# Optimization experiments

Measured on AMD Instinct MI355X. Metric: run time of the kernel, lower is better.

Reference implementation:

```python
import jax, jax.numpy as jnp
import numpy as np

D_MODEL, D_STATE, D_CONV, DT_RANK = 512, 64, 4, 32


def setup_inputs() -> dict:
    key = jax.random.key(0)
    ks = jax.random.split(key, 8)
    Bsz, L = 2, 2048
    s = lambda k, shape: jax.random.normal(k, shape, jnp.float32) * 0.02
    return {
        "x": jax.random.normal(ks[0], (Bsz, L, D_MODEL), jnp.float32),
        "in_proj_w": s(ks[1], (D_MODEL, 2 * D_MODEL)),
        "in_proj_b": jnp.zeros((2 * D_MODEL,), jnp.float32),
        "conv_w": s(ks[2], (D_MODEL, 1, D_CONV)),  # depthwise: [C_out, C_in/groups=1, K]
        "conv_b": jnp.zeros((D_MODEL,), jnp.float32),
        "x_proj_w": s(ks[3], (D_MODEL, DT_RANK + 2 * D_STATE)),
        "x_proj_b": jnp.zeros((DT_RANK + 2 * D_STATE,), jnp.float32),
        "dt_proj_w": s(ks[4], (DT_RANK, D_MODEL)),
        "dt_proj_b": jnp.zeros((D_MODEL,), jnp.float32),
        "A_log": jnp.log(jnp.broadcast_to(
            jnp.arange(1, D_STATE + 1, dtype=jnp.float32), (D_MODEL, D_STATE))),
        "B_param": jax.random.normal(ks[5], (D_MODEL, D_STATE), jnp.float32),
        "C_param": jax.random.normal(ks[6], (D_MODEL, D_STATE), jnp.float32),
        "D_param": jnp.ones((D_MODEL,), jnp.float32),
    }


def reference(x, in_proj_w, in_proj_b, conv_w, conv_b, x_proj_w, x_proj_b,
              dt_proj_w, dt_proj_b, A_log, B_param, C_param, D_param):
    Bsz, L, _ = x.shape
    # in_proj -> split into (x, z)
    xz = x @ in_proj_w + in_proj_b                       # [B, L, 2D]
    xc, z = jnp.split(xz, 2, axis=-1)                    # each [B, L, D]
    # depthwise causal conv1d, padding=K-1 both sides, truncate to L (as in torch)
    y = jax.lax.conv_general_dilated(
        xc.transpose(0, 2, 1), conv_w, window_strides=(1,),
        padding=[(D_CONV - 1, D_CONV - 1)],
        dimension_numbers=("NCH", "OIH", "NCH"),
        feature_group_count=D_MODEL)                     # [B, D, L+K-1]
    xc = (y + conv_b[None, :, None])[:, :, :L].transpose(0, 2, 1)  # [B, L, D]
    # selective parameters
    xp = xc @ x_proj_w + x_proj_b                        # [B, L, dt_rank + 2N]
    dt, Bp, Cp = jnp.split(xp, [DT_RANK, DT_RANK + D_STATE], axis=-1)
    dt = jax.nn.softplus(dt @ dt_proj_w + dt_proj_b)     # [B, L, D]
    A = -jnp.exp(A_log)                                  # [D, N]

    def step(h, ins):
        dt_t, Bp_t, Cp_t, u_t = ins                      # [B,D],[B,N],[B,N],[B,D]
        A_d = jnp.exp(dt_t[..., None] * A)               # [B, D, N]
        B_d = dt_t[..., None] * (B_param * Bp_t[:, None, :])
        h = A_d * h + B_d * u_t[..., None]               # [B, D, N]
        y_t = jnp.sum((C_param * Cp_t[:, None, :]) * h, axis=-1)  # [B, D]
        return h, y_t

    h0 = jnp.zeros((Bsz, D_MODEL, D_STATE), x.dtype)
    xs = (dt.transpose(1, 0, 2), Bp.transpose(1, 0, 2),
          Cp.transpose(1, 0, 2), xc.transpose(1, 0, 2))
    _, ys = jax.lax.scan(step, h0, xs)                   # ys: [L, B, D]
    y = ys.transpose(1, 0, 2) + D_param * xc             # skip connection
    return y * jax.nn.silu(z)                            # gated output [B, L, D]
```

## Files before the change

### kernel.cpp

```cpp
#include <hip/hip_runtime.h>
#include <hip/hip_bf16.h>

#define BSZ 2
#define SEQL 2048
#define DM 512
#define DST 64
#define DCONV 4
#define DTR 32
#define NROWS (BSZ * SEQL)

#define NC 32
#define CL 64

#define XPD_LD 640

typedef unsigned short u16;
typedef short bf16x8 __attribute__((ext_vector_type(8)));
typedef float f32x4 __attribute__((ext_vector_type(4)));

#if __has_builtin(__builtin_amdgcn_exp2f)
#define EXP2(x) __builtin_amdgcn_exp2f(x)
#else
#define EXP2(x) exp2f(x)
#endif
#if __has_builtin(__builtin_amdgcn_logf)
#define LOG2(x) __builtin_amdgcn_logf(x)
#else
#define LOG2(x) log2f(x)
#endif

__device__ __forceinline__ u16 f2bf(float f) {
  unsigned u = __float_as_uint(f);
  return (u16)((u + 0x7FFFu + ((u >> 16) & 1u)) >> 16);
}
__device__ __forceinline__ float bf2f(u16 h) {
  return __uint_as_float(((unsigned)h) << 16);
}

__device__ __forceinline__ void gload_lds16(const u16* g, u16* l) {
  __builtin_amdgcn_global_load_lds(
      (const __attribute__((address_space(1))) void*)(const void*)g,
      (__attribute__((address_space(3))) void*)(void*)l, 16, 0, 0);
}

__global__ __launch_bounds__(256) void split_x_kernel(
    const float* __restrict__ x, u16* __restrict__ hi, u16* __restrict__ lo) {
  int idx = (blockIdx.x * 256 + threadIdx.x) * 4;
  float4 v = *(const float4*)(x + idx);
  ushort4 h, l;
  h.x = f2bf(v.x); l.x = f2bf(v.x - bf2f(h.x));
  h.y = f2bf(v.y); l.y = f2bf(v.y - bf2f(h.y));
  h.z = f2bf(v.z); l.z = f2bf(v.z - bf2f(h.z));
  h.w = f2bf(v.w); l.w = f2bf(v.w - bf2f(h.w));
  *(ushort4*)(hi + idx) = h;
  *(ushort4*)(lo + idx) = l;
}

__global__ __launch_bounds__(256) void split_w_kernel(
    const float* __restrict__ W, u16* __restrict__ Wt_hi,
    u16* __restrict__ Wt_lo) {
  __shared__ u16 shi[32][33], slo[32][33];
  const int n0 = blockIdx.x * 32;
  const int k0 = blockIdx.y * 32;
  const int i = threadIdx.x >> 5;
  const int j = threadIdx.x & 31;
#pragma unroll
  for (int r = 0; r < 4; ++r) {
    int k = i + r * 8;
    float v = W[(size_t)(k0 + k) * 1024 + n0 + j];
    u16 h = f2bf(v);
    shi[k][j] = h;
    slo[k][j] = f2bf(v - bf2f(h));
  }
  __syncthreads();
#pragma unroll
  for (int r = 0; r < 4; ++r) {
    int n = i + r * 8;
    Wt_hi[(size_t)(n0 + n) * 512 + k0 + j] = shi[j][n];
    Wt_lo[(size_t)(n0 + n) * 512 + k0 + j] = slo[j][n];
  }
}

__global__ __launch_bounds__(256) void w_combine_kernel(
    const float* __restrict__ xw, const float* __restrict__ dw,
    u16* __restrict__ Wt_hi, u16* __restrict__ Wt_lo) {
  int idx = blockIdx.x * 256 + threadIdx.x;
  int r = idx >> 9;
  int k = idx & 511;
  float v;
  if (r < 128) {
    v = xw[(size_t)k * 160 + 32 + r];
  } else {
    int d = r - 128;
    float s = 0.f;
#pragma unroll
    for (int j = 0; j < DTR; ++j) s += xw[(size_t)k * 160 + j] * dw[(size_t)j * DM + d];
    v = s;
  }
  u16 h = f2bf(v);
  Wt_hi[idx] = h;
  Wt_lo[idx] = f2bf(v - bf2f(h));
}

__global__ __launch_bounds__(256) void bias_combine_kernel(
    const float* __restrict__ xb, const float* __restrict__ dw,
    const float* __restrict__ db, float* __restrict__ bias_c) {
  int r = blockIdx.x * 256 + threadIdx.x;
  if (r >= 640) return;
  float v;
  if (r < 128) {
    v = xb[32 + r];
  } else {
    int d = r - 128;
    float s = db[d];
#pragma unroll
    for (int j = 0; j < DTR; ++j) s += xb[j] * dw[(size_t)j * DM + d];
    v = s;
  }
  bias_c[r] = v;
}

__global__ __launch_bounds__(256) void mfma_split_gemm(
    const u16* __restrict__ A_hi, const u16* __restrict__ A_lo,
    const u16* __restrict__ Bt_hi, const u16* __restrict__ Bt_lo,
    const float* __restrict__ bias, float* __restrict__ C) {
  __shared__ alignas(16) u16 sAh[4096], sAl[4096], sBh[4096], sBl[4096];

  const int lane = threadIdx.x & 63;
  const int wv = threadIdx.x >> 6;
  const int bm = blockIdx.y * 128;
  const int bn = blockIdx.x * 128;
  const int fr = lane & 15;
  const int q = lane >> 4;

  const int st_rowc = lane >> 2;
  const int st_qd = lane & 3;

  const bf16x8 *pAh[4], *pAl[4], *pBh[4], *pBl[4];
#pragma unroll
  for (int t = 0; t < 4; ++t) {
    int ra = (wv >> 1) * 64 + t * 16 + fr;
    int ea = ra * 32 + ((q ^ ((ra >> 1) & 3)) * 8);
    pAh[t] = (const bf16x8*)(sAh + ea);
    pAl[t] = (const bf16x8*)(sAl + ea);
    int rb = (wv & 1) * 64 + t * 16 + fr;
    int eb = rb * 32 + ((q ^ ((rb >> 1) & 3)) * 8);
    pBh[t] = (const bf16x8*)(sBh + eb);
    pBl[t] = (const bf16x8*)(sBl + eb);
  }

  f32x4 zero = {0.f, 0.f, 0.f, 0.f};
  f32x4 acc[4][4];
#pragma unroll
  for (int i = 0; i < 4; ++i)
#pragma unroll
    for (int j = 0; j < 4; ++j) acc[i][j] = zero;

  auto stage = [&](int k0) {
#pragma unroll
    for (int i = 0; i < 2; ++i) {
      int c = wv + i * 4;
      int row = c * 16 + st_rowc;
      int qs = st_qd ^ ((row >> 1) & 3);
      size_t ga = (size_t)(bm + row) * 512 + k0 + qs * 8;
      size_t gb = (size_t)(bn + row) * 512 + k0 + qs * 8;
      gload_lds16(A_hi + ga, sAh + c * 512);
      gload_lds16(A_lo + ga, sAl + c * 512);
      gload_lds16(Bt_hi + gb, sBh + c * 512);
      gload_lds16(Bt_lo + gb, sBl + c * 512);
    }
  };

  stage(0);
  for (int kt = 0; kt < 16; ++kt) {
    __syncthreads();
    bf16x8 ah[4], al[4], bh[4], bl[4];
#pragma unroll
    for (int t = 0; t < 4; ++t) {
      ah[t] = *pAh[t];
      al[t] = *pAl[t];
      bh[t] = *pBh[t];
      bl[t] = *pBl[t];
    }
    __syncthreads();
    if (kt < 15) stage((kt + 1) * 32);
#pragma unroll
    for (int mi = 0; mi < 4; ++mi)
#pragma unroll
      for (int nj = 0; nj < 4; ++nj) {
        f32x4 a = acc[mi][nj];
        a = __builtin_amdgcn_mfma_f32_16x16x32_bf16(al[mi], bh[nj], a, 0, 0, 0);
        a = __builtin_amdgcn_mfma_f32_16x16x32_bf16(ah[mi], bl[nj], a, 0, 0, 0);
        a = __builtin_amdgcn_mfma_f32_16x16x32_bf16(ah[mi], bh[nj], a, 0, 0, 0);
        acc[mi][nj] = a;
      }
  }

#pragma unroll
  for (int mi = 0; mi < 4; ++mi) {
#pragma unroll
    for (int nj = 0; nj < 4; ++nj) {
      int row = bm + (wv >> 1) * 64 + mi * 16 + q * 4;
      int col = bn + (wv & 1) * 64 + nj * 16 + fr;
      float bs = bias[col];
#pragma unroll
      for (int e = 0; e < 4; ++e)
        C[(size_t)(row + e) * 1024 + col] = acc[mi][nj][e] + bs;
    }
  }
}

__global__ __launch_bounds__(256) void xpd_gemm_kernel(
    const u16* __restrict__ A_hi, const u16* __restrict__ A_lo,
    const u16* __restrict__ Bt_hi, const u16* __restrict__ Bt_lo,
    const float* __restrict__ bias, float* __restrict__ C) {
  __shared__ alignas(16) u16 sBh[64 * 512];
  __shared__ alignas(16) u16 sBl[64 * 512];

  const int lane = threadIdx.x & 63;
  const int wv = threadIdx.x >> 6;
  const int wr = wv >> 1;
  const int wc = wv & 1;
  const int bm = blockIdx.y * 128;
  const int bn = blockIdx.x * 64;
  const int fr = lane & 15;
  const int q = lane >> 4;

  {
    const int r0 = wv * 16;
#pragma unroll
    for (int i = 0; i < 16; ++i) {
      int r = r0 + i;
      size_t g = (size_t)(bn + r) * 512 + (size_t)(lane ^ (r & 7)) * 8;
      gload_lds16(Bt_hi + g, sBh + r * 512);
      gload_lds16(Bt_lo + g, sBl + r * 512);
    }
  }
  __syncthreads();

  size_t arow[4];
#pragma unroll
  for (int mi = 0; mi < 4; ++mi)
    arow[mi] = (size_t)(bm + wr * 64 + mi * 16 + fr) * 512;
  int bcol[2];
#pragma unroll
  for (int nj = 0; nj < 2; ++nj) bcol[nj] = wc * 32 + nj * 16 + fr;

  f32x4 zero = {0.f, 0.f, 0.f, 0.f};
  f32x4 acc[4][2];
#pragma unroll
  for (int i = 0; i < 4; ++i) {
    acc[i][0] = zero;
    acc[i][1] = zero;
  }

#pragma unroll 4
  for (int kt = 0; kt < 16; ++kt) {
    bf16x8 ah[4], al[4], bh[2], bl[2];
    const int kc = kt * 4 + q;
#pragma unroll
    for (int nj = 0; nj < 2; ++nj) {
      int off = bcol[nj] * 512 + ((kc ^ (bcol[nj] & 7)) * 8);
      bh[nj] = *(const bf16x8*)(sBh + off);
      bl[nj] = *(const bf16x8*)(sBl + off);
    }
#pragma unroll
    for (int mi = 0; mi < 4; ++mi) {
      size_t ga = arow[mi] + kt * 32 + q * 8;
      ah[mi] = *(const bf16x8*)(A_hi + ga);
      al[mi] = *(const bf16x8*)(A_lo + ga);
    }
#pragma unroll
    for (int mi = 0; mi < 4; ++mi)
#pragma unroll
      for (int nj = 0; nj < 2; ++nj) {
        f32x4 a = acc[mi][nj];
        a = __builtin_amdgcn_mfma_f32_16x16x32_bf16(al[mi], bh[nj], a, 0, 0, 0);
        a = __builtin_amdgcn_mfma_f32_16x16x32_bf16(ah[mi], bl[nj], a, 0, 0, 0);
        a = __builtin_amdgcn_mfma_f32_16x16x32_bf16(ah[mi], bh[nj], a, 0, 0, 0);
        acc[mi][nj] = a;
      }
  }

  const bool act = (bn >= 128);
#pragma unroll
  for (int mi = 0; mi < 4; ++mi) {
#pragma unroll
    for (int nj = 0; nj < 2; ++nj) {
      int row = bm + wr * 64 + mi * 16 + q * 4;
      int col = bn + wc * 32 + nj * 16 + fr;
      float bs = bias[col];
#pragma unroll
      for (int e = 0; e < 4; ++e) {
        float v = acc[mi][nj][e] + bs;
        if (act) {
          float sp = 0.6931471806f * LOG2(1.f + EXP2(v * 1.44269504f));
          v = (v > 20.f) ? v : sp;
        }
        C[(size_t)(row + e) * XPD_LD + col] = v;
      }
    }
  }
}

__global__ __launch_bounds__(256) void conv_split_kernel(
    const float* __restrict__ xz, const float* __restrict__ w,
    const float* __restrict__ cb, float* __restrict__ xc,
    u16* __restrict__ hi, u16* __restrict__ lo) {
  int idx4 = blockIdx.x * 256 + threadIdx.x;
  if (idx4 >= NROWS * DM / 4) return;
  const int d0 = (idx4 & (DM / 4 - 1)) * 4;
  const int row = idx4 >> 7;
  const int t = row & (SEQL - 1);

  float4 acc = *(const float4*)(cb + d0);
#pragma unroll
  for (int k = 0; k < DCONV; ++k) {
    int ts = t + k - (DCONV - 1);
    if (ts >= 0) {
      float4 v = *(const float4*)(xz + (size_t)(row + k - (DCONV - 1)) * (2 * DM) + d0);
      acc.x += w[(d0 + 0) * DCONV + k] * v.x;
      acc.y += w[(d0 + 1) * DCONV + k] * v.y;
      acc.z += w[(d0 + 2) * DCONV + k] * v.z;
      acc.w += w[(d0 + 3) * DCONV + k] * v.w;
    }
  }
  size_t o = (size_t)row * DM + d0;
  *(float4*)(xc + o) = acc;
  ushort4 h, l;
  h.x = f2bf(acc.x); l.x = f2bf(acc.x - bf2f(h.x));
  h.y = f2bf(acc.y); l.y = f2bf(acc.y - bf2f(h.y));
  h.z = f2bf(acc.z); l.z = f2bf(acc.z - bf2f(h.z));
  h.w = f2bf(acc.w); l.w = f2bf(acc.w - bf2f(h.w));
  *(ushort4*)(hi + o) = h;
  *(ushort4*)(lo + o) = l;
}

__global__ __launch_bounds__(256) void scan_phase1(
    const float* __restrict__ xpd, const float* __restrict__ xc,
    const float* __restrict__ A_log, const float* __restrict__ Bpar,
    float* __restrict__ hout, float* __restrict__ sdt_arr) {
  const int lane = threadIdx.x & 63;
  const int wid = (blockIdx.x << 2) + (threadIdx.x >> 6);
  const int ch = wid >> 5;
  const int c = wid & (NC - 1);
  const int b = ch >> 9;
  const int d = ch & (DM - 1);
  const int n = lane;

  const float aq = -__expf(A_log[d * DST + n]) * 1.44269504f;
  const float bpn = Bpar[d * DST + n];
  float h = 0.f, sdt = 0.f;

  const size_t row0 = (size_t)b * SEQL + (size_t)c * CL;
  const float* dtp = xpd + row0 * XPD_LD + 128 + d;
  const float* up = xc + row0 * DM + d;
  const float* bp = xpd + row0 * XPD_LD + n;

  for (int t0 = 0; t0 < CL; t0 += 4) {
    float dtv[4], uv[4], bpt[4];
#pragma unroll
    for (int j = 0; j < 4; ++j) {
      dtv[j] = dtp[(size_t)(t0 + j) * XPD_LD];
      uv[j] = up[(size_t)(t0 + j) * DM];
      bpt[j] = bp[(size_t)(t0 + j) * XPD_LD];
    }
#pragma unroll
    for (int j = 0; j < 4; ++j) {
      float Ad = EXP2(dtv[j] * aq);
      h = Ad * h + (bpn * bpt[j]) * (dtv[j] * uv[j]);
      sdt += dtv[j];
    }
  }
  hout[(size_t)wid * DST + n] = h;
  if (lane == 0) sdt_arr[wid] = sdt;
}

__global__ __launch_bounds__(256) void scan_phase2(
    const float* __restrict__ A_log, float* __restrict__ hout,
    const float* __restrict__ sdt_arr) {
  const int lane = threadIdx.x & 63;
  const int ch = (blockIdx.x << 2) + (threadIdx.x >> 6);
  const int d = ch & (DM - 1);
  const float aq = -__expf(A_log[d * DST + lane]) * 1.44269504f;

  float tmp[NC], pa[NC];
#pragma unroll
  for (int c = 0; c < NC; ++c) {
    tmp[c] = hout[((size_t)ch * NC + c) * DST + lane];
    pa[c] = EXP2(aq * sdt_arr[ch * NC + c]);
  }
  float h = 0.f;
#pragma unroll
  for (int c = 0; c < NC; ++c) {
    hout[((size_t)ch * NC + c) * DST + lane] = h;
    h = pa[c] * h + tmp[c];
  }
}

__global__ __launch_bounds__(256) void scan_phase3(
    const float* __restrict__ xpd, const float* __restrict__ xc,
    const float* __restrict__ xz,
    const float* __restrict__ A_log, const float* __restrict__ Bpar,
    const float* __restrict__ Cpar, const float* __restrict__ Dpar,
    const float* __restrict__ hin, float* __restrict__ out) {
  __shared__ float W[4][16][68];

  const int lane = threadIdx.x & 63;
  const int wave = threadIdx.x >> 6;
  const int wid = (blockIdx.x << 2) + wave;
  const int ch = wid >> 5;
  const int c = wid & (NC - 1);
  const int b = ch >> 9;
  const int d = ch & (DM - 1);
  const int n = lane;

  const float aq = -__expf(A_log[d * DST + n]) * 1.44269504f;
  const float bpn = Bpar[d * DST + n];
  const float cpn = Cpar[d * DST + n];
  const float Dd = Dpar[d];
  float h = hin[(size_t)wid * DST + n];

  const size_t row0 = (size_t)b * SEQL + (size_t)c * CL;
  const float* dtp = xpd + row0 * XPD_LD + 128 + d;
  const float* up = xc + row0 * DM + d;
  const float* bp = xpd + row0 * XPD_LD + n;
  const float* cp = xpd + row0 * XPD_LD + 64 + n;

  const int tt = lane & 15;
  const int q = lane >> 4;

  for (int t0 = 0; t0 < CL; t0 += 16) {
#pragma unroll
    for (int g = 0; g < 16; g += 4) {
      float dtv[4], uv[4], bpt[4], cpt[4];
#pragma unroll
      for (int j = 0; j < 4; ++j) {
        size_t t = (size_t)(t0 + g + j);
        dtv[j] = dtp[t * XPD_LD];
        uv[j] = up[t * DM];
        bpt[j] = bp[t * XPD_LD];
        cpt[j] = cp[t * XPD_LD];
      }
#pragma unroll
      for (int j = 0; j < 4; ++j) {
        float Ad = EXP2(dtv[j] * aq);
        h = Ad * h + (bpn * bpt[j]) * (dtv[j] * uv[j]);
        W[wave][g + j][n] = (cpn * cpt[j]) * h;
      }
    }
    const float4* wr = (const float4*)&W[wave][tt][q * 16];
    float s = 0.f;
#pragma unroll
    for (int k2 = 0; k2 < 4; ++k2) {
      float4 v = wr[k2];
      s += (v.x + v.y) + (v.z + v.w);
    }
    s += __shfl_xor(s, 16, 64);
    s += __shfl_xor(s, 32, 64);
    if (lane < 16) {
      size_t t = (size_t)(t0 + lane);
      float u = up[t * DM];
      float zz = xz[(row0 + t) * (2 * DM) + DM + d];
      float y = s + Dd * u;
      float sil = zz / (1.f + __expf(-zz));
      out[(row0 + t) * DM + d] = y * sil;
    }
  }
}

extern "C" void kernel_launch(void* const* d_in, const int* in_sizes, int n_in,
                              void* d_out, int out_size, void* d_ws,
                              size_t ws_size, hipStream_t stream) {
  const float* x = (const float*)d_in[0];
  const float* in_proj_w = (const float*)d_in[1];
  const float* in_proj_b = (const float*)d_in[2];
  const float* conv_w = (const float*)d_in[3];
  const float* conv_b = (const float*)d_in[4];
  const float* x_proj_w = (const float*)d_in[5];
  const float* x_proj_b = (const float*)d_in[6];
  const float* dt_proj_w = (const float*)d_in[7];
  const float* dt_proj_b = (const float*)d_in[8];
  const float* A_log = (const float*)d_in[9];
  const float* B_param = (const float*)d_in[10];
  const float* C_param = (const float*)d_in[11];
  const float* D_param = (const float*)d_in[12];
  float* out = (float*)d_out;

  float* ws = (float*)d_ws;
  float* xz = ws;
  float* xc = xz + (size_t)NROWS * 2 * DM;
  float* xpd = xc + (size_t)NROWS * DM;
  float* hout = xpd + (size_t)NROWS * XPD_LD;
  float* sdt = hout + (size_t)BSZ * DM * NC * DST;
  float* bias_c = sdt + (size_t)BSZ * DM * NC;
  u16* A_hi = (u16*)(bias_c + 1024);
  u16* A_lo = A_hi + (size_t)NROWS * DM;
  u16* Wt_in_hi = A_lo + (size_t)NROWS * DM;
  u16* Wt_in_lo = Wt_in_hi + (size_t)1024 * 512;
  u16* Wt_c_hi = Wt_in_lo + (size_t)1024 * 512;
  u16* Wt_c_lo = Wt_c_hi + (size_t)640 * 512;

  hipLaunchKernelGGL(split_x_kernel, dim3((NROWS * DM) / (256 * 4)), dim3(256),
                     0, stream, x, A_hi, A_lo);
  hipLaunchKernelGGL(split_w_kernel, dim3(32, 16), dim3(256), 0, stream,
                     in_proj_w, Wt_in_hi, Wt_in_lo);
  hipLaunchKernelGGL(w_combine_kernel, dim3((640 * 512) / 256), dim3(256), 0,
                     stream, x_proj_w, dt_proj_w, Wt_c_hi, Wt_c_lo);
  hipLaunchKernelGGL(bias_combine_kernel, dim3(3), dim3(256), 0, stream,
                     x_proj_b, dt_proj_w, dt_proj_b, bias_c);

  hipLaunchKernelGGL(mfma_split_gemm, dim3(1024 / 128, NROWS / 128),
                     dim3(256), 0, stream, A_hi, A_lo, Wt_in_hi, Wt_in_lo,
                     in_proj_b, xz);

  hipLaunchKernelGGL(conv_split_kernel, dim3((NROWS * DM / 4 + 255) / 256),
                     dim3(256), 0, stream, xz, conv_w, conv_b, xc, A_hi, A_lo);

  hipLaunchKernelGGL(xpd_gemm_kernel, dim3(640 / 64, NROWS / 128),
                     dim3(256), 0, stream, A_hi, A_lo, Wt_c_hi, Wt_c_lo,
                     bias_c, xpd);

  {
    dim3 grid((BSZ * DM * NC) / 4);
    hipLaunchKernelGGL(scan_phase1, grid, dim3(256), 0, stream,
                       xpd, xc, A_log, B_param, hout, sdt);
    hipLaunchKernelGGL(scan_phase2, dim3((BSZ * DM) / 4), dim3(256), 0, stream,
                       A_log, hout, sdt);
    hipLaunchKernelGGL(scan_phase3, grid, dim3(256), 0, stream,
                       xpd, xc, xz, A_log, B_param, C_param, D_param,
                       hout, out);
  }
}
```

Before: 247.4 us.

## Keep in_proj weight tile resident in LDS and stream A from global

Result: slower. 265.4 us (+7.3%).

```diff
diff --git a/kernel.cpp b/kernel.cpp
--- a/kernel.cpp
+++ b/kernel.cpp
@@ -120,74 +120,70 @@
   bias_c[r] = v;
 }
 
-__global__ __launch_bounds__(256) void mfma_split_gemm(
+__global__ __launch_bounds__(256) void in_proj_resident_kernel(
     const u16* __restrict__ A_hi, const u16* __restrict__ A_lo,
     const u16* __restrict__ Bt_hi, const u16* __restrict__ Bt_lo,
     const float* __restrict__ bias, float* __restrict__ C) {
-  __shared__ alignas(16) u16 sAh[4096], sAl[4096], sBh[4096], sBl[4096];
+  __shared__ alignas(16) u16 sBh[64 * 512];
+  __shared__ alignas(16) u16 sBl[64 * 512];
 
   const int lane = threadIdx.x & 63;
   const int wv = threadIdx.x >> 6;
+  const int wr = wv >> 1;
+  const int wc = wv & 1;
   const int bm = blockIdx.y * 128;
-  const int bn = blockIdx.x * 128;
+  const int bn = blockIdx.x * 64;
   const int fr = lane & 15;
   const int q = lane >> 4;
 
-  const int st_rowc = lane >> 2;
-  const int st_qd = lane & 3;
-
-  const bf16x8 *pAh[4], *pAl[4], *pBh[4], *pBl[4];
-#pragma unroll
-  for (int t = 0; t < 4; ++t) {
-    int ra = (wv >> 1) * 64 + t * 16 + fr;
-    int ea = ra * 32 + ((q ^ ((ra >> 1) & 3)) * 8);
-    pAh[t] = (const bf16x8*)(sAh + ea);
-    pAl[t] = (const bf16x8*)(sAl + ea);
-    int rb = (wv & 1) * 64 + t * 16 + fr;
-    int eb = rb * 32 + ((q ^ ((rb >> 1) & 3)) * 8);
-    pBh[t] = (const bf16x8*)(sBh + eb);
-    pBl[t] = (const bf16x8*)(sBl + eb);
-  }
+  {
+    const int r0 = wv * 16;
+#pragma unroll
+    for (int i = 0; i < 16; ++i) {
+      int r = r0 + i;
+      size_t g = (size_t)(bn + r) * 512 + (size_t)(lane ^ (r & 7)) * 8;
+      gload_lds16(Bt_hi + g, sBh + r * 512);
+      gload_lds16(Bt_lo + g, sBl + r * 512);
+    }
+  }
+  __syncthreads();
+
+  size_t arow[4];
+#pragma unroll
+  for (int mi = 0; mi < 4; ++mi)
+    arow[mi] = (size_t)(bm + wr * 64 + mi * 16 + fr) * 512;
+  int bcol[2];
+#pragma unroll
+  for (int nj = 0; nj < 2; ++nj) bcol[nj] = wc * 32 + nj * 16 + fr;
 
   f32x4 zero = {0.f, 0.f, 0.f, 0.f};
-  f32x4 acc[4][4];
-#pragma unroll
-  for (int i = 0; i < 4; ++i)
-#pragma unroll
-    for (int j = 0; j < 4; ++j) acc[i][j] = zero;
-
-  auto stage = [&](int k0) {
-#pragma unroll
-    for (int i = 0; i < 2; ++i) {
-      int c = wv + i * 4;
-      int row = c * 16 + st_rowc;
-      int qs = st_qd ^ ((row >> 1) & 3);
-      size_t ga = (size_t)(bm + row) * 512 + k0 + qs * 8;
-      size_t gb = (size_t)(bn + row) * 512 + k0 + qs * 8;
-      gload_lds16(A_hi + ga, sAh + c * 512);
-      gload_lds16(A_lo + ga, sAl + c * 512);
-      gload_lds16(Bt_hi + gb, sBh + c * 512);
-      gload_lds16(Bt_lo + gb, sBl + c * 512);
-    }
-  };
-
-  stage(0);
+  f32x4 acc[4][2];
+#pragma unroll
+  for (int i = 0; i < 4; ++i) {
+    acc[i][0] = zero;
+    acc[i][1] = zero;
+  }
+
+#pragma unroll 4
   for (int kt = 0; kt < 16; ++kt) {
-    __syncthreads();
-    bf16x8 ah[4], al[4], bh[4], bl[4];
-#pragma unroll
-    for (int t = 0; t < 4; ++t) {
-      ah[t] = *pAh[t];
-      al[t] = *pAl[t];
-      bh[t] = *pBh[t];
-      bl[t] = *pBl[t];
-    }
-    __syncthreads();
-    if (kt < 15) stage((kt + 1) * 32);
+    bf16x8 ah[4], al[4], bh[2], bl[2];
+    const int kc = kt * 4 + q;
+#pragma unroll
+    for (int nj = 0; nj < 2; ++nj) {
+      int off = bcol[nj] * 512 + ((kc ^ (bcol[nj] & 7)) * 8);
+      bh[nj] = *(const bf16x8*)(sBh + off);
+      bl[nj] = *(const bf16x8*)(sBl + off);
+    }
+#pragma unroll
+    for (int mi = 0; mi < 4; ++mi) {
+      size_t ga = arow[mi] + kt * 32 + q * 8;
+      ah[mi] = *(const bf16x8*)(A_hi + ga);
+      al[mi] = *(const bf16x8*)(A_lo + ga);
+    }
 #pragma unroll
     for (int mi = 0; mi < 4; ++mi)
 #pragma unroll
-      for (int nj = 0; nj < 4; ++nj) {
+      for (int nj = 0; nj < 2; ++nj) {
         f32x4 a = acc[mi][nj];
         a = __builtin_amdgcn_mfma_f32_16x16x32_bf16(al[mi], bh[nj], a, 0, 0, 0);
         a = __builtin_amdgcn_mfma_f32_16x16x32_bf16(ah[mi], bl[nj], a, 0, 0, 0);
@@ -199,9 +195,9 @@
 #pragma unroll
   for (int mi = 0; mi < 4; ++mi) {
 #pragma unroll
-    for (int nj = 0; nj < 4; ++nj) {
-      int row = bm + (wv >> 1) * 64 + mi * 16 + q * 4;
-      int col = bn + (wv & 1) * 64 + nj * 16 + fr;
+    for (int nj = 0; nj < 2; ++nj) {
+      int row = bm + wr * 64 + mi * 16 + q * 4;
+      int col = bn + wc * 32 + nj * 16 + fr;
       float bs = bias[col];
 #pragma unroll
       for (int e = 0; e < 4; ++e)
@@ -510,7 +506,7 @@
   hipLaunchKernelGGL(bias_combine_kernel, dim3(3), dim3(256), 0, stream,
                      x_proj_b, dt_proj_w, dt_proj_b, bias_c);
 
-  hipLaunchKernelGGL(mfma_split_gemm, dim3(1024 / 128, NROWS / 128),
+  hipLaunchKernelGGL(in_proj_resident_kernel, dim3(1024 / 64, NROWS / 128),
                      dim3(256), 0, stream, A_hi, A_lo, Wt_in_hi, Wt_in_lo,
                      in_proj_b, xz);
 
```
